# Optimization experiments

Hardware: AMD Instinct MI355X
Metric: run time of the kernel (lower is better)

Reference implementation:

```python
import jax, jax.numpy as jnp
import numpy as np
from jax import lax

B, D, N, C = 8, 1, 12288, 256
H = 8            # num_heads
WS = 64          # window size (pixels per window)
HID = 1024       # mlp hidden = 4*C
K = 9            # conv kernel size
EPS = 1e-5


def setup_inputs() -> dict:
    key = jax.random.key(0)
    ks = jax.random.split(key, 8)
    w = lambda i, shape: jax.random.normal(ks[i], shape, jnp.float32) * 0.02
    return {
        "x": jax.random.normal(ks[0], (B, D, N, C), jnp.float32),
        "ln1_g": jnp.ones((C,), jnp.float32),
        "ln1_b": jnp.zeros((C,), jnp.float32),
        "conv_w": w(1, (C, C, K)),            # OIH layout (out_ch, in_ch, k)
        "conv_b": jnp.zeros((C,), jnp.float32),
        "qkv_w": w(2, (C, 3 * C)),            # stored (in, out): y = x @ W + b
        "qkv_b": jnp.zeros((3 * C,), jnp.float32),
        "proj_w": w(3, (C, C)),
        "proj_b": jnp.zeros((C,), jnp.float32),
        "ln2_g": jnp.ones((C,), jnp.float32),
        "ln2_b": jnp.zeros((C,), jnp.float32),
        "fc1_w": w(4, (C, HID)),
        "fc1_b": jnp.zeros((HID,), jnp.float32),
        "fc2_w": w(5, (HID, C)),
        "fc2_b": jnp.zeros((C,), jnp.float32),
    }


def _layernorm(x, g, b):
    mu = jnp.mean(x, axis=-1, keepdims=True)
    var = jnp.mean(jnp.square(x - mu), axis=-1, keepdims=True)
    return (x - mu) * lax.rsqrt(var + EPS) * g + b


def reference(x, ln1_g, ln1_b, conv_w, conv_b, qkv_w, qkv_b,
              proj_w, proj_b, ln2_g, ln2_b, fc1_w, fc1_b, fc2_w, fc2_b):
    shortcut = x                                  # (B, D, N, C)
    h = _layernorm(x, ln1_g, ln1_b)

    # Conv1d over pixel dim N, channels C, same padding
    hc = h.reshape(B * D, N, C).transpose(0, 2, 1)            # (BD, C, N)
    hc = lax.conv_general_dilated(
        hc, conv_w, window_strides=(1,), padding=[((K - 1) // 2, (K - 1) // 2)],
        dimension_numbers=("NCH", "OIH", "NCH"))
    hc = hc + conv_b[None, :, None]
    h = hc.transpose(0, 2, 1).reshape(B, D, N, C)

    # Window partition (no shift): (B*D*N/WS, WS, C)
    win = h.reshape(-1, WS, C)
    hd = C // H
    qkv = (win @ qkv_w + qkv_b).reshape(-1, WS, 3, H, hd)
    q = qkv[:, :, 0].transpose(0, 2, 1, 3)        # (nW, H, WS, hd)
    k = qkv[:, :, 1].transpose(0, 2, 1, 3)
    v = qkv[:, :, 2].transpose(0, 2, 1, 3)
    scale = hd ** (-0.5)
    attn = jnp.einsum("whqd,whkd->whqk", q * scale, k)
    attn = jax.nn.softmax(attn, axis=-1)
    out = jnp.einsum("whqk,whkd->whqd", attn, v)
    out = out.transpose(0, 2, 1, 3).reshape(-1, WS, C)
    out = out @ proj_w + proj_b

    h = out.reshape(B, D, N, C)
    x1 = shortcut + h                             # residual 1
    mlp_in = _layernorm(x1, ln2_g, ln2_b)
    mlp = jax.nn.gelu(mlp_in @ fc1_w + fc1_b, approximate=False) @ fc2_w + fc2_b
    return x1 + mlp                               # residual 2
```

## Files before the change

kernel.cpp:

```cpp
#include <hip/hip_runtime.h>

#define DEVI __device__ __forceinline__

typedef __attribute__((ext_vector_type(4))) float  f32x4;
typedef __attribute__((ext_vector_type(8))) short  s16x8;
typedef __attribute__((ext_vector_type(4))) short  s16x4;
typedef __attribute__((ext_vector_type(8))) __bf16 bf16x8;

constexpr int  Nn  = 12288;
constexpr int  NP  = 12296;
constexpr long TOK = 98304;

DEVI short f2bf(float f) {
  unsigned u = __builtin_bit_cast(unsigned, f);
  u += 0x7fffu + ((u >> 16) & 1u);
  return (short)(u >> 16);
}

DEVI f32x4 MFMA(s16x8 a, s16x8 b, f32x4 c) {
  return __builtin_amdgcn_mfma_f32_16x16x32_bf16(
      __builtin_bit_cast(bf16x8, a), __builtin_bit_cast(bf16x8, b), c, 0, 0, 0);
}

DEVI void gld16(const void* g, void* l) {
  __builtin_amdgcn_global_load_lds(
      (const __attribute__((address_space(1))) void*)g,
      (__attribute__((address_space(3))) void*)l, 16, 0, 0);
}

template <int CNT, int NT>
DEVI void stageG(const short* __restrict__ g_base, long g_row0, int ld, int k0,
                 short* __restrict__ lds, int tid) {
  const int w = tid >> 6;
#pragma unroll
  for (int c = 0; c < CNT; ++c) {
    const int u = c * NT + tid;
    const int row = u >> 3, ch = u & 7;
    const short* g = g_base + (g_row0 + row) * (long)ld + k0 + ch * 8;
    gld16(g, lds + (c * NT + w * 64) * 8);
  }
}

DEVI void xcd_decode(int W, int total, int ncol, long& row0, int& col0) {
  const int per = total >> 3;
  const int L = (W & 7) * per + (W >> 3);
  row0 = (long)(L / ncol) * 128;
  col0 = (L % ncol) * 128;
}

__global__ void prep_k(const float* __restrict__ qkv_w, const float* __restrict__ proj_w,
                       const float* __restrict__ fc1_w, const float* __restrict__ fc2_w,
                       const float* __restrict__ conv_w,
                       short* __restrict__ qkvWt, short* __restrict__ projWt,
                       short* __restrict__ fc1Wt, short* __restrict__ fc2Wt,
                       short* __restrict__ convWt, short* __restrict__ hp) {
  int idx = blockIdx.x * 256 + threadIdx.x;
  if (idx < 196608) {
    int o = idx >> 8, i = idx & 255;
    qkvWt[idx] = f2bf(qkv_w[i * 768 + o]);
    return;
  }
  idx -= 196608;
  if (idx < 65536) {
    int o = idx >> 8, i = idx & 255;
    projWt[idx] = f2bf(proj_w[i * 256 + o]);
    return;
  }
  idx -= 65536;
  if (idx < 262144) {
    int o = idx >> 8, i = idx & 255;
    fc1Wt[idx] = f2bf(fc1_w[i * 1024 + o]);
    return;
  }
  idx -= 262144;
  if (idx < 262144) {
    int o = idx >> 10, i = idx & 1023;
    fc2Wt[idx] = f2bf(fc2_w[i * 256 + o]);
    return;
  }
  idx -= 262144;
  if (idx < 589824) {
    int co = idx / 2304, rem = idx % 2304;
    int k = rem >> 8, ci = rem & 255;
    convWt[idx] = f2bf(conv_w[co * 2304 + ci * 9 + k]);
    return;
  }
  idx -= 589824;
  if (idx < 16384) {
    int b = idx >> 11, rem = idx & 2047;
    int rs = rem >> 8, ch = rem & 255;
    int p = rs < 4 ? rs : 12288 + rs;
    hp[((long)b * NP + p) * 256 + ch] = 0;
  }
}

__global__ __launch_bounds__(256) void ln_k(const float* __restrict__ x,
                                            const float* __restrict__ gw,
                                            const float* __restrict__ bw,
                                            short* __restrict__ out) {
  const int tid = threadIdx.x, w = tid >> 6, lane = tid & 63;
  const long t = (long)blockIdx.x * 4 + w;
  f32x4 v = *((const f32x4*)(x + t * 256) + lane);
  float s  = v[0] + v[1] + v[2] + v[3];
  float ss = v[0] * v[0] + v[1] * v[1] + v[2] * v[2] + v[3] * v[3];
#pragma unroll
  for (int mk = 1; mk < 64; mk <<= 1) {
    s  += __shfl_xor(s, mk);
    ss += __shfl_xor(ss, mk);
  }
  const float mu   = s * (1.0f / 256.0f);
  const float var  = ss * (1.0f / 256.0f) - mu * mu;
  const float rstd = rsqrtf(var + 1e-5f);
  f32x4 g4 = *((const f32x4*)gw + lane);
  f32x4 b4 = *((const f32x4*)bw + lane);
  const long orow = t + (t / Nn) * 8 + 4;
  s16x4 o4;
#pragma unroll
  for (int j = 0; j < 4; ++j) o4[j] = f2bf((v[j] - mu) * rstd * g4[j] + b4[j]);
  *((s16x4*)(out + orow * 256) + lane) = o4;
}

template <int EPI>
__global__ __launch_bounds__(256, 2) void gemm_k(
    const short* __restrict__ A, int lda,
    const short* __restrict__ Bt,
    const float* __restrict__ bias,
    const float* res, short* outS, float* outF,
    int ldo, int K, int ncol) {
  __shared__ __align__(16) short As[2][128][64];
  __shared__ __align__(16) short Bs[2][128][64];
  const int tid = threadIdx.x, w = tid >> 6, lane = tid & 63;
  const int q = lane >> 4, r16 = lane & 15;
  long row0; int col0;
  xcd_decode(blockIdx.x, gridDim.x, ncol, row0, col0);
  const int wr = w >> 1, wc = w & 1;
  f32x4 acc[4][4] = {};

  stageG<4, 256>(A, row0, lda, 0, &As[0][0][0], tid);
  stageG<4, 256>(Bt, col0, K, 0, &Bs[0][0][0], tid);
  __syncthreads();
  int cur = 0;
  for (int k0 = 0; k0 < K; k0 += 64) {
    if (k0 + 64 < K) {
      stageG<4, 256>(A, row0, lda, k0 + 64, &As[cur ^ 1][0][0], tid);
      stageG<4, 256>(Bt, col0, K, k0 + 64, &Bs[cur ^ 1][0][0], tid);
    }
#pragma unroll
    for (int kk = 0; kk < 2; ++kk) {
      s16x8 af[4], bfv[4];
#pragma unroll
      for (int m = 0; m < 4; ++m) af[m] = *(const s16x8*)&As[cur][wr * 64 + m * 16 + r16][kk * 32 + q * 8];
#pragma unroll
      for (int n = 0; n < 4; ++n) bfv[n] = *(const s16x8*)&Bs[cur][wc * 64 + n * 16 + r16][kk * 32 + q * 8];
#pragma unroll
      for (int m = 0; m < 4; ++m)
#pragma unroll
        for (int n = 0; n < 4; ++n) acc[m][n] = MFMA(af[m], bfv[n], acc[m][n]);
    }
    __syncthreads();
    cur ^= 1;
  }

  const long orow = row0 + wr * 64;
  const int  ocol = col0 + wc * 64;
#pragma unroll
  for (int n = 0; n < 4; ++n) {
    const int   gc = ocol + n * 16 + r16;
    const float bn = bias[gc];
#pragma unroll
    for (int m = 0; m < 4; ++m) {
      const long gr = orow + m * 16 + q * 4;
#pragma unroll
      for (int r = 0; r < 4; ++r) {
        float v = acc[m][n][r] + bn;
        const long o = (gr + r) * (long)ldo + gc;
        if constexpr (EPI == 0) {
          outS[o] = f2bf(v);
        } else if constexpr (EPI == 1) {
          outF[o] = v + res[o];
        } else {
          float t = 0.5f * v * (1.0f + erff(v * 0.70710678118654752f));
          outS[o] = f2bf(t);
        }
      }
    }
  }
}

__global__ __launch_bounds__(256, 2) void conv_k(const short* __restrict__ hp,
                                                 const short* __restrict__ convWt,
                                                 const float* __restrict__ bias,
                                                 short* __restrict__ out) {
  __shared__ __align__(16) short As[160][64];
  __shared__ __align__(16) short Bs[2][128][64];
  const int tid = threadIdx.x, w = tid >> 6, lane = tid & 63;
  const int q = lane >> 4, r16 = lane & 15;
  long row0; int col0;
  xcd_decode(blockIdx.x, gridDim.x, 2, row0, col0);
  const int  b  = (int)(row0 / Nn);
  const int  n0 = (int)(row0 % Nn);
  const long abase = (long)b * NP + n0;
  const int  wr = w >> 1, wc = w & 1;
  f32x4 acc[4][4] = {};

  stageG<5, 256>(hp, abase, 256, 0, &As[0][0], tid);
  stageG<4, 256>(convWt, col0, 2304, 0, &Bs[0][0][0], tid);
  __syncthreads();
  int cur = 0;
  for (int k0 = 0; k0 < 256; k0 += 64) {
    for (int tap = 0; tap < 9; ++tap) {
      if (tap < 8)
        stageG<4, 256>(convWt, col0, 2304, (tap + 1) * 256 + k0, &Bs[cur ^ 1][0][0], tid);
      else if (k0 + 64 < 256)
        stageG<4, 256>(convWt, col0, 2304, k0 + 64, &Bs[cur ^ 1][0][0], tid);
#pragma unroll
      for (int kk = 0; kk < 2; ++kk) {
        s16x8 af[4], bfv[4];
#pragma unroll
        for (int m = 0; m < 4; ++m)
          af[m] = *(const s16x8*)&As[tap + wr * 64 + m * 16 + r16][kk * 32 + q * 8];
#pragma unroll
        for (int n = 0; n < 4; ++n)
          bfv[n] = *(const s16x8*)&Bs[cur][wc * 64 + n * 16 + r16][kk * 32 + q * 8];
#pragma unroll
        for (int m = 0; m < 4; ++m)
#pragma unroll
          for (int n = 0; n < 4; ++n) acc[m][n] = MFMA(af[m], bfv[n], acc[m][n]);
      }
      __syncthreads();
      cur ^= 1;
    }
    if (k0 + 64 < 256) {
      stageG<5, 256>(hp, abase, 256, k0 + 64, &As[0][0], tid);
      __syncthreads();
    }
  }

  const long orow = row0 + wr * 64;
  const int  ocol = col0 + wc * 64;
#pragma unroll
  for (int n = 0; n < 4; ++n) {
    const int   gc = ocol + n * 16 + r16;
    const float bn = bias[gc];
#pragma unroll
    for (int m = 0; m < 4; ++m) {
      const long gr = orow + m * 16 + q * 4;
#pragma unroll
      for (int r = 0; r < 4; ++r) out[(gr + r) * 256L + gc] = f2bf(acc[m][n][r] + bn);
    }
  }
}

__global__ __launch_bounds__(512, 4) void proj_ln_k(
    const short* __restrict__ A,
    const short* __restrict__ Bt,
    const float* __restrict__ bias,
    const float* __restrict__ res,
    const float* __restrict__ gw, const float* __restrict__ bw,
    float* __restrict__ x1,
    short* __restrict__ lnout) {
  __shared__ __align__(16) short As[128][64];
  __shared__ __align__(16) short Bs[256][64];
  __shared__ float red[4][128][2];
  const int tid = threadIdx.x, w = tid >> 6, lane = tid & 63;
  const int q = lane >> 4, r16 = lane & 15;
  const int W = blockIdx.x, per = gridDim.x >> 3;
  const long row0 = (long)((W & 7) * per + (W >> 3)) * 128;
  const int wr = w >> 2, wc = w & 3;
  f32x4 acc[4][4] = {};

  for (int k0 = 0; k0 < 256; k0 += 64) {
    stageG<2, 512>(A, row0, 256, k0, &As[0][0], tid);
    stageG<4, 512>(Bt, 0, 256, k0, &Bs[0][0], tid);
    __syncthreads();
#pragma unroll
    for (int kk = 0; kk < 2; ++kk) {
      s16x8 af[4], bfv[4];
#pragma unroll
      for (int m = 0; m < 4; ++m) af[m] = *(const s16x8*)&As[wr * 64 + m * 16 + r16][kk * 32 + q * 8];
#pragma unroll
      for (int n = 0; n < 4; ++n) bfv[n] = *(const s16x8*)&Bs[wc * 64 + n * 16 + r16][kk * 32 + q * 8];
#pragma unroll
      for (int m = 0; m < 4; ++m)
#pragma unroll
        for (int n = 0; n < 4; ++n) acc[m][n] = MFMA(af[m], bfv[n], acc[m][n]);
    }
    __syncthreads();
  }

  float biasr[4], gv[4], bv[4];
#pragma unroll
  for (int n = 0; n < 4; ++n) {
    const int gc = wc * 64 + n * 16 + r16;
    biasr[n] = bias[gc]; gv[n] = gw[gc]; bv[n] = bw[gc];
  }

#pragma unroll
  for (int m = 0; m < 4; ++m) {
#pragma unroll
    for (int r = 0; r < 4; ++r) {
      const long gr = row0 + wr * 64 + m * 16 + q * 4 + r;
      float s = 0.f, ss = 0.f;
#pragma unroll
      for (int n = 0; n < 4; ++n) {
        const int gc = wc * 64 + n * 16 + r16;
        float v = acc[m][n][r] + biasr[n] + res[gr * 256 + gc];
        acc[m][n][r] = v;
        x1[gr * 256 + gc] = v;
        s += v; ss += v * v;
      }
#pragma unroll
      for (int mk = 1; mk < 16; mk <<= 1) {
        s  += __shfl_xor(s, mk);
        ss += __shfl_xor(ss, mk);
      }
      if (r16 == 0) {
        const int lr = wr * 64 + m * 16 + q * 4 + r;
        red[wc][lr][0] = s;
        red[wc][lr][1] = ss;
      }
    }
  }
  __syncthreads();

#pragma unroll
  for (int m = 0; m < 4; ++m) {
#pragma unroll
    for (int r = 0; r < 4; ++r) {
      const int  lr = wr * 64 + m * 16 + q * 4 + r;
      const long gr = row0 + lr;
      const float S  = red[0][lr][0] + red[1][lr][0] + red[2][lr][0] + red[3][lr][0];
      const float SS = red[0][lr][1] + red[1][lr][1] + red[2][lr][1] + red[3][lr][1];
      const float mu = S * (1.0f / 256.0f);
      const float rstd = rsqrtf(SS * (1.0f / 256.0f) - mu * mu + 1e-5f);
#pragma unroll
      for (int n = 0; n < 4; ++n) {
        const int gc = wc * 64 + n * 16 + r16;
        lnout[gr * 256 + gc] = f2bf((acc[m][n][r] - mu) * rstd * gv[n] + bv[n]);
      }
    }
  }
}

__global__ __launch_bounds__(256, 2) void attn_k(const short* __restrict__ qkv,
                                                 short* __restrict__ o) {
  __shared__ __align__(16) short Pt[4][64][68];
  __shared__ __align__(16) short Vs[4][64][32];
  const int tid = threadIdx.x, w = tid >> 6, lane = tid & 63;
  const int q = lane >> 4, r16 = lane & 15;
  const int job = blockIdx.x * 4 + w;
  const int win = job >> 3, h = job & 7;
  const short* base = qkv + (long)win * 64 * 768;

#pragma unroll
  for (int c = 0; c < 4; ++c) {
    const int idx16 = c * 64 + lane;
    const short* g = base + (long)(idx16 >> 2) * 768 + 512 + h * 32 + (idx16 & 3) * 8;
    gld16(g, (char*)&Vs[w][0][0] + c * 1024);
  }

  s16x8 aq[4], bk[4];
#pragma unroll
  for (int m = 0; m < 4; ++m)
    aq[m] = *(const s16x8*)(base + (long)(m * 16 + r16) * 768 + h * 32 + q * 8);
#pragma unroll
  for (int n = 0; n < 4; ++n)
    bk[n] = *(const s16x8*)(base + (long)(n * 16 + r16) * 768 + 256 + h * 32 + q * 8);
  f32x4 sc[4][4] = {};
#pragma unroll
  for (int m = 0; m < 4; ++m)
#pragma unroll
    for (int n = 0; n < 4; ++n) sc[m][n] = MFMA(aq[m], bk[n], sc[m][n]);

  const float scale = 0.17677669529663687f;
#pragma unroll
  for (int m = 0; m < 4; ++m) {
#pragma unroll
    for (int r = 0; r < 4; ++r) {
      float a0 = sc[m][0][r] * scale, a1 = sc[m][1][r] * scale;
      float a2 = sc[m][2][r] * scale, a3 = sc[m][3][r] * scale;
      float mx = fmaxf(fmaxf(a0, a1), fmaxf(a2, a3));
      mx = fmaxf(mx, __shfl_xor(mx, 1));
      mx = fmaxf(mx, __shfl_xor(mx, 2));
      mx = fmaxf(mx, __shfl_xor(mx, 4));
      mx = fmaxf(mx, __shfl_xor(mx, 8));
      float e0 = __expf(a0 - mx), e1 = __expf(a1 - mx);
      float e2 = __expf(a2 - mx), e3 = __expf(a3 - mx);
      float sm = e0 + e1 + e2 + e3;
      sm += __shfl_xor(sm, 1);
      sm += __shfl_xor(sm, 2);
      sm += __shfl_xor(sm, 4);
      sm += __shfl_xor(sm, 8);
      float inv = 1.0f / sm;
      sc[m][0][r] = e0 * inv; sc[m][1][r] = e1 * inv;
      sc[m][2][r] = e2 * inv; sc[m][3][r] = e3 * inv;
    }
  }

#pragma unroll
  for (int m = 0; m < 4; ++m)
#pragma unroll
    for (int n = 0; n < 4; ++n) {
      s16x4 p4;
#pragma unroll
      for (int r = 0; r < 4; ++r) p4[r] = f2bf(sc[m][n][r]);
      *(s16x4*)&Pt[w][n * 16 + r16][m * 16 + q * 4] = p4;
    }

  asm volatile("s_waitcnt vmcnt(0)" ::: "memory");

  f32x4 oa[4][2] = {};
#pragma unroll
  for (int ks = 0; ks < 2; ++ks) {
    s16x8 bv[2];
#pragma unroll
    for (int nt = 0; nt < 2; ++nt)
#pragma unroll
      for (int jj = 0; jj < 8; ++jj)
        bv[nt][jj] = Vs[w][ks * 32 + q * 8 + jj][nt * 16 + r16];
#pragma unroll
    for (int m = 0; m < 4; ++m) {
      s16x8 ap;
#pragma unroll
      for (int jj = 0; jj < 8; ++jj)
        ap[jj] = Pt[w][ks * 32 + q * 8 + jj][m * 16 + r16];
#pragma unroll
      for (int nt = 0; nt < 2; ++nt) oa[m][nt] = MFMA(ap, bv[nt], oa[m][nt]);
    }
  }

  short* ob = o + (long)win * 64 * 256 + h * 32;
#pragma unroll
  for (int m = 0; m < 4; ++m)
#pragma unroll
    for (int nt = 0; nt < 2; ++nt)
#pragma unroll
      for (int r = 0; r < 4; ++r)
        ob[(long)(m * 16 + q * 4 + r) * 256 + nt * 16 + r16] = f2bf(oa[m][nt][r]);
}

extern "C" void kernel_launch(void* const* d_in, const int* in_sizes, int n_in,
                              void* d_out, int out_size, void* d_ws, size_t ws_size,
                              hipStream_t stream) {
  const float* x      = (const float*)d_in[0];
  const float* ln1_g  = (const float*)d_in[1];
  const float* ln1_b  = (const float*)d_in[2];
  const float* conv_w = (const float*)d_in[3];
  const float* conv_b = (const float*)d_in[4];
  const float* qkv_w  = (const float*)d_in[5];
  const float* qkv_b  = (const float*)d_in[6];
  const float* proj_w = (const float*)d_in[7];
  const float* proj_b = (const float*)d_in[8];
  const float* ln2_g  = (const float*)d_in[9];
  const float* ln2_b  = (const float*)d_in[10];
  const float* fc1_w  = (const float*)d_in[11];
  const float* fc1_b  = (const float*)d_in[12];
  const float* fc2_w  = (const float*)d_in[13];
  const float* fc2_b  = (const float*)d_in[14];
  float* out = (float*)d_out;

  constexpr long HPsz = (long)8 * NP * 256;
  constexpr long Qsz  = TOK * 768;
  constexpr long Csz  = TOK * 256;
  short* ws    = (short*)d_ws;
  short* hp    = ws;
  short* qkvB  = ws + HPsz;
  short* cvB   = ws + HPsz + Qsz;
  short* hidB  = qkvB;
  short* wts   = ws + HPsz + Qsz + Csz;
  short* qkvWt  = wts;
  short* projWt = qkvWt + 196608;
  short* fc1Wt  = projWt + 65536;
  short* fc2Wt  = fc1Wt + 262144;
  short* convWt = fc2Wt + 262144;

  prep_k<<<5440, 256, 0, stream>>>(qkv_w, proj_w, fc1_w, fc2_w, conv_w,
                                   qkvWt, projWt, fc1Wt, fc2Wt, convWt, hp);
  ln_k<<<24576, 256, 0, stream>>>(x, ln1_g, ln1_b, hp);
  conv_k<<<1536, 256, 0, stream>>>(hp, convWt, conv_b, cvB);
  gemm_k<0><<<4608, 256, 0, stream>>>(cvB, 256, qkvWt, qkv_b,
                                      nullptr, qkvB, nullptr, 768, 256, 6);
  attn_k<<<3072, 256, 0, stream>>>(qkvB, hp);
  proj_ln_k<<<768, 512, 0, stream>>>(hp, projWt, proj_b, x, ln2_g, ln2_b, out, hp);
  gemm_k<2><<<6144, 256, 0, stream>>>(hp, 256, fc1Wt, fc1_b,
                                      nullptr, hidB, nullptr, 1024, 256, 8);
  gemm_k<1><<<1536, 256, 0, stream>>>(hidB, 1024, fc2Wt, fc2_b,
                                      out, nullptr, out, 256, 1024, 2);
}
```

Before: 722.5 us.

## Use triple-buffered K=32 GEMM pipeline with XOR-swizzled LDS and single barrier

```diff
diff --git a/kernel.cpp b/kernel.cpp
--- a/kernel.cpp
+++ b/kernel.cpp
@@ -38,6 +38,18 @@
     const int row = u >> 3, ch = u & 7;
     const short* g = g_base + (g_row0 + row) * (long)ld + k0 + ch * 8;
     gld16(g, lds + (c * NT + w * 64) * 8);
+  }
+}
+
+DEVI void stage32(const short* __restrict__ g_base, long g_row0, int ld, int k0,
+                  short* __restrict__ lds, int tid) {
+#pragma unroll
+  for (int c = 0; c < 2; ++c) {
+    const int u = c * 256 + tid;
+    const int row = u >> 2;
+    const int ch = (u & 3) ^ (row & 3);
+    gld16(g_base + (g_row0 + row) * (long)ld + k0 + ch * 8,
+          lds + ((c * 256 + (tid >> 6) * 64)) * 8);
   }
 }
 
@@ -121,44 +133,67 @@
 }
 
 template <int EPI>
-__global__ __launch_bounds__(256, 2) void gemm_k(
+__global__ __launch_bounds__(256, 3) void gemm3_k(
     const short* __restrict__ A, int lda,
     const short* __restrict__ Bt,
     const float* __restrict__ bias,
     const float* res, short* outS, float* outF,
     int ldo, int K, int ncol) {
-  __shared__ __align__(16) short As[2][128][64];
-  __shared__ __align__(16) short Bs[2][128][64];
+  __shared__ __align__(16) short As[3][128 * 32];
+  __shared__ __align__(16) short Bs[3][128 * 32];
   const int tid = threadIdx.x, w = tid >> 6, lane = tid & 63;
   const int q = lane >> 4, r16 = lane & 15;
   long row0; int col0;
   xcd_decode(blockIdx.x, gridDim.x, ncol, row0, col0);
   const int wr = w >> 1, wc = w & 1;
+  const int sw = q ^ (r16 & 3);
   f32x4 acc[4][4] = {};
 
-  stageG<4, 256>(A, row0, lda, 0, &As[0][0][0], tid);
-  stageG<4, 256>(Bt, col0, K, 0, &Bs[0][0][0], tid);
-  __syncthreads();
-  int cur = 0;
-  for (int k0 = 0; k0 < K; k0 += 64) {
-    if (k0 + 64 < K) {
-      stageG<4, 256>(A, row0, lda, k0 + 64, &As[cur ^ 1][0][0], tid);
-      stageG<4, 256>(Bt, col0, K, k0 + 64, &Bs[cur ^ 1][0][0], tid);
-    }
-#pragma unroll
-    for (int kk = 0; kk < 2; ++kk) {
+  const int nk = K >> 5;
+  stage32(A, row0, lda, 0, As[0], tid);
+  stage32(Bt, col0, K, 0, Bs[0], tid);
+  stage32(A, row0, lda, 32, As[1], tid);
+  stage32(Bt, col0, K, 32, Bs[1], tid);
+
+  int b0 = 0, b1 = 1, b2 = 2;
+  for (int t = 0; t < nk - 1; ++t) {
+    asm volatile("s_waitcnt vmcnt(4)" ::: "memory");
+    __builtin_amdgcn_s_barrier();
+    asm volatile("" ::: "memory");
+    if (t + 2 < nk) {
+      stage32(A, row0, lda, (t + 2) * 32, As[b2], tid);
+      stage32(Bt, col0, K, (t + 2) * 32, Bs[b2], tid);
+    }
+    {
       s16x8 af[4], bfv[4];
 #pragma unroll
-      for (int m = 0; m < 4; ++m) af[m] = *(const s16x8*)&As[cur][wr * 64 + m * 16 + r16][kk * 32 + q * 8];
-#pragma unroll
-      for (int n = 0; n < 4; ++n) bfv[n] = *(const s16x8*)&Bs[cur][wc * 64 + n * 16 + r16][kk * 32 + q * 8];
-#pragma unroll
       for (int m = 0; m < 4; ++m)
+        af[m] = *(const s16x8*)(As[b0] + ((wr * 64 + m * 16 + r16) * 4 + sw) * 8);
+#pragma unroll
+      for (int n = 0; n < 4; ++n)
+        bfv[n] = *(const s16x8*)(Bs[b0] + ((wc * 64 + n * 16 + r16) * 4 + sw) * 8);
+#pragma unroll
+      for (int m = 0; m < 4; ++m)
 #pragma unroll
         for (int n = 0; n < 4; ++n) acc[m][n] = MFMA(af[m], bfv[n], acc[m][n]);
     }
-    __syncthreads();
-    cur ^= 1;
+    const int tmp = b0; b0 = b1; b1 = b2; b2 = tmp;
+  }
+  asm volatile("s_waitcnt vmcnt(0)" ::: "memory");
+  __builtin_amdgcn_s_barrier();
+  asm volatile("" ::: "memory");
+  {
+    s16x8 af[4], bfv[4];
+#pragma unroll
+    for (int m = 0; m < 4; ++m)
+      af[m] = *(const s16x8*)(As[b0] + ((wr * 64 + m * 16 + r16) * 4 + sw) * 8);
+#pragma unroll
+    for (int n = 0; n < 4; ++n)
+      bfv[n] = *(const s16x8*)(Bs[b0] + ((wc * 64 + n * 16 + r16) * 4 + sw) * 8);
+#pragma unroll
+    for (int m = 0; m < 4; ++m)
+#pragma unroll
+      for (int n = 0; n < 4; ++n) acc[m][n] = MFMA(af[m], bfv[n], acc[m][n]);
   }
 
   const long orow = row0 + wr * 64;
@@ -478,12 +513,12 @@
                                    qkvWt, projWt, fc1Wt, fc2Wt, convWt, hp);
   ln_k<<<24576, 256, 0, stream>>>(x, ln1_g, ln1_b, hp);
   conv_k<<<1536, 256, 0, stream>>>(hp, convWt, conv_b, cvB);
-  gemm_k<0><<<4608, 256, 0, stream>>>(cvB, 256, qkvWt, qkv_b,
-                                      nullptr, qkvB, nullptr, 768, 256, 6);
+  gemm3_k<0><<<4608, 256, 0, stream>>>(cvB, 256, qkvWt, qkv_b,
+                                       nullptr, qkvB, nullptr, 768, 256, 6);
   attn_k<<<3072, 256, 0, stream>>>(qkvB, hp);
   proj_ln_k<<<768, 512, 0, stream>>>(hp, projWt, proj_b, x, ln2_g, ln2_b, out, hp);
-  gemm_k<2><<<6144, 256, 0, stream>>>(hp, 256, fc1Wt, fc1_b,
-                                      nullptr, hidB, nullptr, 1024, 256, 8);
-  gemm_k<1><<<1536, 256, 0, stream>>>(hidB, 1024, fc2Wt, fc2_b,
-                                      out, nullptr, out, 256, 1024, 2);
-}
+  gemm3_k<2><<<6144, 256, 0, stream>>>(hp, 256, fc1Wt, fc1_b,
+                                       nullptr, hidB, nullptr, 1024, 256, 8);
+  gemm3_k<1><<<1536, 256, 0, stream>>>(hidB, 1024, fc2Wt, fc2_b,
+                                       out, nullptr, out, 256, 1024, 2);
+}
```

Result: faster. 677.7 us (-6.2%).

## Widen GEMM N-tiles and drop LDS double buffering for linear layers

Applied to the files above, without the earlier changes.

```diff
diff --git a/kernel.cpp b/kernel.cpp
--- a/kernel.cpp
+++ b/kernel.cpp
@@ -41,11 +41,11 @@
   }
 }
 
-DEVI void xcd_decode(int W, int total, int ncol, long& row0, int& col0) {
+DEVI void xcd_decode(int W, int total, int ncol, long& row0, int& col0, int bn) {
   const int per = total >> 3;
   const int L = (W & 7) * per + (W >> 3);
   row0 = (long)(L / ncol) * 128;
-  col0 = (L % ncol) * 128;
+  col0 = (L % ncol) * bn;
 }
 
 __global__ void prep_k(const float* __restrict__ qkv_w, const float* __restrict__ proj_w,
@@ -120,51 +120,49 @@
   *((s16x4*)(out + orow * 256) + lane) = o4;
 }
 
-template <int EPI>
-__global__ __launch_bounds__(256, 2) void gemm_k(
+template <int WN, int EPI>
+__global__ __launch_bounds__(256, 2) void gemmF_k(
     const short* __restrict__ A, int lda,
     const short* __restrict__ Bt,
     const float* __restrict__ bias,
     const float* res, short* outS, float* outF,
     int ldo, int K, int ncol) {
-  __shared__ __align__(16) short As[2][128][64];
-  __shared__ __align__(16) short Bs[2][128][64];
+  constexpr int BN = WN * 2;
+  constexpr int NF = WN / 16;
+  __shared__ __align__(16) short As[128][64];
+  __shared__ __align__(16) short Bs[BN][64];
   const int tid = threadIdx.x, w = tid >> 6, lane = tid & 63;
   const int q = lane >> 4, r16 = lane & 15;
   long row0; int col0;
-  xcd_decode(blockIdx.x, gridDim.x, ncol, row0, col0);
+  xcd_decode(blockIdx.x, gridDim.x, ncol, row0, col0, BN);
   const int wr = w >> 1, wc = w & 1;
-  f32x4 acc[4][4] = {};
-
-  stageG<4, 256>(A, row0, lda, 0, &As[0][0][0], tid);
-  stageG<4, 256>(Bt, col0, K, 0, &Bs[0][0][0], tid);
-  __syncthreads();
-  int cur = 0;
+  f32x4 acc[4][NF] = {};
+
   for (int k0 = 0; k0 < K; k0 += 64) {
-    if (k0 + 64 < K) {
-      stageG<4, 256>(A, row0, lda, k0 + 64, &As[cur ^ 1][0][0], tid);
-      stageG<4, 256>(Bt, col0, K, k0 + 64, &Bs[cur ^ 1][0][0], tid);
-    }
+    stageG<4, 256>(A, row0, lda, k0, &As[0][0], tid);
+    stageG<BN / 32, 256>(Bt, col0, K, k0, &Bs[0][0], tid);
+    __syncthreads();
 #pragma unroll
     for (int kk = 0; kk < 2; ++kk) {
-      s16x8 af[4], bfv[4];
-#pragma unroll
-      for (int m = 0; m < 4; ++m) af[m] = *(const s16x8*)&As[cur][wr * 64 + m * 16 + r16][kk * 32 + q * 8];
-#pragma unroll
-      for (int n = 0; n < 4; ++n) bfv[n] = *(const s16x8*)&Bs[cur][wc * 64 + n * 16 + r16][kk * 32 + q * 8];
+      s16x8 af[4], bfv[NF];
 #pragma unroll
       for (int m = 0; m < 4; ++m)
-#pragma unroll
-        for (int n = 0; n < 4; ++n) acc[m][n] = MFMA(af[m], bfv[n], acc[m][n]);
+        af[m] = *(const s16x8*)&As[wr * 64 + m * 16 + r16][kk * 32 + q * 8];
+#pragma unroll
+      for (int n = 0; n < NF; ++n)
+        bfv[n] = *(const s16x8*)&Bs[wc * WN + n * 16 + r16][kk * 32 + q * 8];
+#pragma unroll
+      for (int m = 0; m < 4; ++m)
+#pragma unroll
+        for (int n = 0; n < NF; ++n) acc[m][n] = MFMA(af[m], bfv[n], acc[m][n]);
     }
     __syncthreads();
-    cur ^= 1;
   }
 
   const long orow = row0 + wr * 64;
-  const int  ocol = col0 + wc * 64;
-#pragma unroll
-  for (int n = 0; n < 4; ++n) {
+  const int  ocol = col0 + wc * WN;
+#pragma unroll
+  for (int n = 0; n < NF; ++n) {
     const int   gc = ocol + n * 16 + r16;
     const float bn = bias[gc];
 #pragma unroll
@@ -196,7 +194,7 @@
   const int tid = threadIdx.x, w = tid >> 6, lane = tid & 63;
   const int q = lane >> 4, r16 = lane & 15;
   long row0; int col0;
-  xcd_decode(blockIdx.x, gridDim.x, 2, row0, col0);
+  xcd_decode(blockIdx.x, gridDim.x, 2, row0, col0, 128);
   const int  b  = (int)(row0 / Nn);
   const int  n0 = (int)(row0 % Nn);
   const long abase = (long)b * NP + n0;
@@ -478,12 +476,12 @@
                                    qkvWt, projWt, fc1Wt, fc2Wt, convWt, hp);
   ln_k<<<24576, 256, 0, stream>>>(x, ln1_g, ln1_b, hp);
   conv_k<<<1536, 256, 0, stream>>>(hp, convWt, conv_b, cvB);
-  gemm_k<0><<<4608, 256, 0, stream>>>(cvB, 256, qkvWt, qkv_b,
-                                      nullptr, qkvB, nullptr, 768, 256, 6);
+  gemmF_k<96, 0><<<3072, 256, 0, stream>>>(cvB, 256, qkvWt, qkv_b,
+                                           nullptr, qkvB, nullptr, 768, 256, 4);
   attn_k<<<3072, 256, 0, stream>>>(qkvB, hp);
   proj_ln_k<<<768, 512, 0, stream>>>(hp, projWt, proj_b, x, ln2_g, ln2_b, out, hp);
-  gemm_k<2><<<6144, 256, 0, stream>>>(hp, 256, fc1Wt, fc1_b,
-                                      nullptr, hidB, nullptr, 1024, 256, 8);
-  gemm_k<1><<<1536, 256, 0, stream>>>(hidB, 1024, fc2Wt, fc2_b,
-                                      out, nullptr, out, 256, 1024, 2);
-}
+  gemmF_k<128, 2><<<3072, 256, 0, stream>>>(hp, 256, fc1Wt, fc1_b,
+                                            nullptr, hidB, nullptr, 1024, 256, 4);
+  gemmF_k<128, 1><<<768, 256, 0, stream>>>(hidB, 1024, fc2Wt, fc2_b,
+                                           out, nullptr, out, 256, 1024, 1);
+}
```

New measurement: 715.1 us. No clear change (-1.0%).
